# Kernel optimization log

Measured on AMD Instinct MI355X. Metric: run time of the kernel, lower is better.

Reference implementation:

```python
import jax, jax.numpy as jnp
import numpy as np

N_HEADS = 4
ROPE_THETA = 10000.0


def rotate_half(x):
    h = x.shape[-1] // 2
    return jnp.concatenate([-x[..., h:], x[..., :h]], axis=-1)


def setup_inputs() -> dict:
    key = jax.random.key(0)
    k1, k2, k3, k4, k5 = jax.random.split(key, 5)
    B, L, D, M = 4, 2048, 216, 64
    x = jax.random.normal(k1, (B, L, D), dtype=jnp.float32)
    mem_k = jax.random.normal(k2, (B, M, D), dtype=jnp.float32)
    mem_v = jax.random.normal(k3, (B, M, D), dtype=jnp.float32)
    attention_mask = jnp.ones((B, L), dtype=jnp.int32)
    # pre-transposed Linear weights (y = x @ W); scaled for stability
    Wqkv = jax.random.normal(k4, (D, 3 * D), dtype=jnp.float32) * (D ** -0.5)
    Wo = jax.random.normal(k5, (D, D), dtype=jnp.float32) * (D ** -0.5)
    return {"x": x, "mem_k": mem_k, "mem_v": mem_v,
            "attention_mask": attention_mask, "Wqkv": Wqkv, "Wo": Wo}


def reference(x, mem_k, mem_v, attention_mask, Wqkv, Wo):
    B, L, D = x.shape
    H = N_HEADS
    hd = D // H
    scale = hd ** -0.5
    M = mem_k.shape[1]

    # QKV projection -> [B, L, 3, H, hd] -> [B, H, L, hd]
    qkv = (x @ Wqkv).reshape(B, L, 3, H, hd)
    q = jnp.transpose(qkv[:, :, 0], (0, 2, 1, 3))
    k = jnp.transpose(qkv[:, :, 1], (0, 2, 1, 3))
    v = jnp.transpose(qkv[:, :, 2], (0, 2, 1, 3))

    # RoPE (cos/sin: [L, hd], broadcast over B,H)
    inv_freq = 1.0 / (ROPE_THETA ** (jnp.arange(0, hd, 2, dtype=jnp.float32) / hd))
    t = jnp.arange(L, dtype=jnp.float32)
    freqs = jnp.outer(t, inv_freq)
    emb = jnp.concatenate([freqs, freqs], axis=-1)
    cos, sin = jnp.cos(emb), jnp.sin(emb)
    q = q * cos + rotate_half(q) * sin
    k = k * cos + rotate_half(k) * sin

    # memory KV: [B, M, D] -> [B, H, M, hd], prepend along kv axis
    mk = jnp.transpose(mem_k.reshape(B, M, H, hd), (0, 2, 1, 3))
    mv = jnp.transpose(mem_v.reshape(B, M, H, hd), (0, 2, 1, 3))
    k_all = jnp.concatenate([mk, k], axis=2)  # [B, H, M+L, hd]
    v_all = jnp.concatenate([mv, v], axis=2)

    scores = jnp.einsum('bhld,bhmd->bhlm', q, k_all) * scale  # [B,H,L,M+L]

    # causal mask applies only to the self-attention block (cols >= M)
    causal = jnp.triu(jnp.ones((L, L), dtype=bool), k=1)
    full_causal = jnp.concatenate([jnp.zeros((L, M), dtype=bool), causal], axis=1)
    scores = jnp.where(full_causal[None, None], -jnp.inf, scores)

    # padding mask: memory positions always valid
    combined = jnp.concatenate(
        [jnp.ones((B, M), dtype=attention_mask.dtype), attention_mask], axis=-1)
    scores = jnp.where(combined[:, None, None, :] == 0, -jnp.inf, scores)

    attn = jax.nn.softmax(scores, axis=-1)  # dropout is identity in eval
    out = jnp.einsum('bhlm,bhmd->bhld', attn, v_all)
    out = jnp.transpose(out, (0, 2, 1, 3)).reshape(B, L, D)
    return out @ Wo
```

## Files before the change

kernel.cpp:

```cpp
#include <hip/hip_runtime.h>
#include <math.h>

#define B_ 4
#define L_ 2048
#define D_ 216
#define H_ 4
#define HD 54
#define HDP 64
#define M_ 64
#define LK 2112
#define NT_ 33
#define KP 256
#define SPB 84
#define QSCALE 0.19632593f

typedef __attribute__((ext_vector_type(8))) __bf16 bf16x8;
typedef __attribute__((ext_vector_type(4))) __bf16 bf16x4;
typedef __attribute__((ext_vector_type(4))) float f32x4;

__device__ __forceinline__ int unpack_d(int j) { return (j >> 1) + 27 * (j & 1); }

__global__ __launch_bounds__(256) void prep(const float* __restrict__ Wqkv,
                                            const float* __restrict__ Wo,
                                            const int* __restrict__ amask,
                                            const float* __restrict__ mk,
                                            const float* __restrict__ mv,
                                            __bf16* __restrict__ wqkvt,
                                            __bf16* __restrict__ wot,
                                            float2* __restrict__ table,
                                            float* __restrict__ bias,
                                            int* __restrict__ padflag,
                                            __bf16* __restrict__ kall,
                                            __bf16* __restrict__ vt) {
    const int bid = blockIdx.x, tid = threadIdx.x;
    if (bid < 768) {
        int idx = bid * 256 + tid;
        int pc = idx >> 8, k = idx & 255;
        float v = 0.f;
        if (k < 216) {
            int col = -1;
            if (pc < 256) { int h = pc >> 6, j = pc & 63;
                if (j < HD) col = h * HD + unpack_d(j); }
            else if (pc < 512) { int h = (pc - 256) >> 6, j = (pc - 256) & 63;
                if (j < HD) col = 216 + h * HD + unpack_d(j); }
            else if (pc < 728) col = 432 + (pc - 512);
            if (col >= 0) v = Wqkv[(size_t)k * 648 + col];
        }
        wqkvt[idx] = (__bf16)v;
    } else if (bid < 1024) {
        int idx = (bid - 768) * 256 + tid;
        int n = idx >> 8, k = idx & 255;
        wot[idx] = (__bf16)((n < 216 && k < 216) ? Wo[(size_t)k * 216 + n] : 0.f);
    } else if (bid < 1280) {
        int idx = (bid - 1024) * 256 + tid;
        int l = idx >> 5, ii = idx & 31;
        float2 sc = {0.f, 0.f};
        if (ii < 27) {
            float ang = (float)l * exp2f(-0.49213749924f * (float)ii);
            sc.x = sinf(ang); sc.y = cosf(ang);
        }
        table[idx] = sc;
    } else if (bid < 1313) {
        int idx = (bid - 1280) * 256 + tid;
        if (idx < B_ * LK) {
            int b = idx / LK, c = idx % LK;
            bias[idx] = (c < M_ || amask[b * L_ + c - M_] != 0) ? 0.f : -1e30f;
        }
    } else if (bid == 1313) {
        if (tid < B_ * NT_) {
            int b = tid / NT_, tile = tid % NT_;
            int flag = 0;
            for (int u = 0; u < 64; ++u) {
                int c = tile * 64 + u;
                if (c >= M_ && c < LK && amask[b * L_ + c - M_] == 0) flag = 1;
            }
            padflag[tid] = flag;
        }
    } else {
        int idx = (bid - 1314) * 256 + tid;
        int b  = idx >> 14;
        int m  = (idx >> 8) & 63;
        int h  = (idx >> 6) & 3;
        int dd = idx & 63;
        float kv = (dd < HD) ? mk[((size_t)(b * M_ + m)) * D_ + h * HD + unpack_d(dd)] : 0.f;
        kall[((size_t)(b * 4 + h) * LK + m) * HDP + dd] = (__bf16)kv;
        if (dd < HD)
            vt[((size_t)(b * 4 + h) * HD + dd) * LK + m] =
                (__bf16)mv[((size_t)(b * M_ + m)) * D_ + h * HD + dd];
    }
}

__global__ __launch_bounds__(256) void gemm_qkv(const float* __restrict__ x,
                                                const __bf16* __restrict__ Bt,
                                                const float2* __restrict__ table,
                                                __bf16* __restrict__ qb,
                                                __bf16* __restrict__ kall,
                                                __bf16* __restrict__ vt) {
    __shared__ __align__(16) __bf16 As[8192];
    __shared__ __align__(16) __bf16 Bs[4096];
    const int col0 = blockIdx.x * 64;
    const int row0 = blockIdx.y * 128;
    const int tid = threadIdx.x;
    const int lane = tid & 63;
    const int w = tid >> 6, wm = w >> 1, wn = w & 1;
    const int l15 = lane & 15, l4 = lane >> 4;

    f32x4 acc[4][2];
    #pragma unroll
    for (int m = 0; m < 4; ++m)
        #pragma unroll
        for (int n = 0; n < 2; ++n) acc[m][n] = (f32x4){0.f, 0.f, 0.f, 0.f};

    float4 rfa[4][2];
    bf16x8 rb[2];
    #pragma unroll
    for (int i = 0; i < 4; ++i) { int c = tid + 256 * i, r = c >> 3, c8 = c & 7;
        int k = c8 * 8;
        rfa[i][0] = *reinterpret_cast<const float4*>(x + (size_t)(row0 + r) * 216 + k);
        rfa[i][1] = *reinterpret_cast<const float4*>(x + (size_t)(row0 + r) * 216 + k + 4); }
    #pragma unroll
    for (int i = 0; i < 2; ++i) { int c = tid + 256 * i, r = c >> 3, c8 = c & 7;
        rb[i] = *reinterpret_cast<const bf16x8*>(Bt + (size_t)(col0 + r) * KP + c8 * 8); }

    for (int kit = 0; kit < 4; ++kit) {
        __syncthreads();
        #pragma unroll
        for (int i = 0; i < 4; ++i) { int c = tid + 256 * i, r = c >> 3, c8 = c & 7;
            bf16x8 v;
            #pragma unroll
            for (int j = 0; j < 4; ++j) { v[j] = (__bf16)rfa[i][0][j]; v[4 + j] = (__bf16)rfa[i][1][j]; }
            *reinterpret_cast<bf16x8*>(&As[r * 64 + ((c8 ^ (r & 7)) * 8)]) = v; }
        #pragma unroll
        for (int i = 0; i < 2; ++i) { int c = tid + 256 * i, r = c >> 3, c8 = c & 7;
            *reinterpret_cast<bf16x8*>(&Bs[r * 64 + ((c8 ^ (r & 7)) * 8)]) = rb[i]; }
        __syncthreads();
        if (kit < 3) {
            const int k0 = (kit + 1) * 64;
            #pragma unroll
            for (int i = 0; i < 4; ++i) { int c = tid + 256 * i, r = c >> 3, c8 = c & 7;
                int k = k0 + c8 * 8;
                if (k < 216) {
                    rfa[i][0] = *reinterpret_cast<const float4*>(x + (size_t)(row0 + r) * 216 + k);
                    rfa[i][1] = *reinterpret_cast<const float4*>(x + (size_t)(row0 + r) * 216 + k + 4);
                } else {
                    rfa[i][0] = (float4){0.f, 0.f, 0.f, 0.f};
                    rfa[i][1] = (float4){0.f, 0.f, 0.f, 0.f};
                } }
            #pragma unroll
            for (int i = 0; i < 2; ++i) { int c = tid + 256 * i, r = c >> 3, c8 = c & 7;
                rb[i] = *reinterpret_cast<const bf16x8*>(Bt + (size_t)(col0 + r) * KP + k0 + c8 * 8); }
        }
        #pragma unroll
        for (int ks = 0; ks < 2; ++ks) {
            bf16x8 af[4], bfr[2];
            #pragma unroll
            for (int m = 0; m < 4; ++m) { int row = wm * 64 + m * 16 + l15; int ch = ks * 4 + l4;
                af[m] = *reinterpret_cast<const bf16x8*>(&As[row * 64 + ((ch ^ (row & 7)) * 8)]); }
            #pragma unroll
            for (int n = 0; n < 2; ++n) { int row = wn * 32 + n * 16 + l15; int ch = ks * 4 + l4;
                bfr[n] = *reinterpret_cast<const bf16x8*>(&Bs[row * 64 + ((ch ^ (row & 7)) * 8)]); }
            #pragma unroll
            for (int m = 0; m < 4; ++m)
                #pragma unroll
                for (int n = 0; n < 2; ++n)
                    acc[m][n] = __builtin_amdgcn_mfma_f32_16x16x32_bf16(af[m], bfr[n], acc[m][n], 0, 0, 0);
        }
    }

    #pragma unroll
    for (int m = 0; m < 4; ++m)
        #pragma unroll
        for (int n = 0; n < 2; ++n) {
            const int cc = col0 + wn * 32 + n * 16 + l15;
            const int rowb = row0 + wm * 64 + m * 16 + l4 * 4;
            const int b = rowb >> 11;
            const int lbase = rowb & 2047;
            if (cc < 512) {
                const bool isq = cc < 256;
                const int h = (cc >> 6) & 3, j = cc & 63;
                const int half = j & 1, ii = j >> 1;
                #pragma unroll
                for (int rr = 0; rr < 4; ++rr) {
                    float me = acc[m][n][rr];
                    float pr = __shfl_xor(me, 1);
                    float2 sc = table[(lbase + rr) * 32 + ii];
                    float v = me * sc.y + (half ? pr * sc.x : -pr * sc.x);
                    if (isq) {
                        qb[((size_t)(b * 4 + h) * L_ + lbase + rr) * HDP + j] =
                            (__bf16)(v * QSCALE);
                    } else {
                        kall[((size_t)(b * 4 + h) * LK + M_ + lbase + rr) * HDP + j] =
                            (__bf16)v;
                    }
                }
            } else if (cc < 728) {
                const int dp = cc - 512;
                const int h = (dp * 1214) >> 16;
                const int d = dp - h * 54;
                #pragma unroll
                for (int rr = 0; rr < 4; ++rr)
                    vt[((size_t)(b * 4 + h) * HD + d) * LK + M_ + lbase + rr] =
                        (__bf16)acc[m][n][rr];
            }
        }
}

__global__ __launch_bounds__(256) void gemm_out(const __bf16* __restrict__ A,
                                                const __bf16* __restrict__ Bt,
                                                float* __restrict__ C, int N) {
    __shared__ __align__(16) __bf16 As[8192];
    __shared__ __align__(16) __bf16 Bs[4096];
    const int col0 = blockIdx.x * 64;
    const int row0 = blockIdx.y * 128;
    const int tid = threadIdx.x;
    const int lane = tid & 63;
    const int w = tid >> 6, wm = w >> 1, wn = w & 1;
    const int l15 = lane & 15, l4 = lane >> 4;

    f32x4 acc[4][2];
    #pragma unroll
    for (int m = 0; m < 4; ++m)
        #pragma unroll
        for (int n = 0; n < 2; ++n) acc[m][n] = (f32x4){0.f, 0.f, 0.f, 0.f};

    bf16x8 ra[4], rb[2];
    #pragma unroll
    for (int i = 0; i < 4; ++i) { int c = tid + 256 * i, r = c >> 3, c8 = c & 7;
        ra[i] = *reinterpret_cast<const bf16x8*>(A + (size_t)(row0 + r) * KP + c8 * 8); }
    #pragma unroll
    for (int i = 0; i < 2; ++i) { int c = tid + 256 * i, r = c >> 3, c8 = c & 7;
        rb[i] = *reinterpret_cast<const bf16x8*>(Bt + (size_t)(col0 + r) * KP + c8 * 8); }

    for (int kit = 0; kit < 4; ++kit) {
        __syncthreads();
        #pragma unroll
        for (int i = 0; i < 4; ++i) { int c = tid + 256 * i, r = c >> 3, c8 = c & 7;
            *reinterpret_cast<bf16x8*>(&As[r * 64 + ((c8 ^ (r & 7)) * 8)]) = ra[i]; }
        #pragma unroll
        for (int i = 0; i < 2; ++i) { int c = tid + 256 * i, r = c >> 3, c8 = c & 7;
            *reinterpret_cast<bf16x8*>(&Bs[r * 64 + ((c8 ^ (r & 7)) * 8)]) = rb[i]; }
        __syncthreads();
        if (kit < 3) {
            const int k0 = (kit + 1) * 64;
            #pragma unroll
            for (int i = 0; i < 4; ++i) { int c = tid + 256 * i, r = c >> 3, c8 = c & 7;
                ra[i] = *reinterpret_cast<const bf16x8*>(A + (size_t)(row0 + r) * KP + k0 + c8 * 8); }
            #pragma unroll
            for (int i = 0; i < 2; ++i) { int c = tid + 256 * i, r = c >> 3, c8 = c & 7;
                rb[i] = *reinterpret_cast<const bf16x8*>(Bt + (size_t)(col0 + r) * KP + k0 + c8 * 8); }
        }
        #pragma unroll
        for (int ks = 0; ks < 2; ++ks) {
            bf16x8 af[4], bfr[2];
            #pragma unroll
            for (int m = 0; m < 4; ++m) { int row = wm * 64 + m * 16 + l15; int ch = ks * 4 + l4;
                af[m] = *reinterpret_cast<const bf16x8*>(&As[row * 64 + ((ch ^ (row & 7)) * 8)]); }
            #pragma unroll
            for (int n = 0; n < 2; ++n) { int row = wn * 32 + n * 16 + l15; int ch = ks * 4 + l4;
                bfr[n] = *reinterpret_cast<const bf16x8*>(&Bs[row * 64 + ((ch ^ (row & 7)) * 8)]); }
            #pragma unroll
            for (int m = 0; m < 4; ++m)
                #pragma unroll
                for (int n = 0; n < 2; ++n)
                    acc[m][n] = __builtin_amdgcn_mfma_f32_16x16x32_bf16(af[m], bfr[n], acc[m][n], 0, 0, 0);
        }
    }
    #pragma unroll
    for (int m = 0; m < 4; ++m)
        #pragma unroll
        for (int n = 0; n < 2; ++n) {
            int cc = col0 + wn * 32 + n * 16 + l15;
            if (cc < N) {
                #pragma unroll
                for (int rr = 0; rr < 4; ++rr)
                    C[(size_t)(row0 + wm * 64 + m * 16 + l4 * 4 + rr) * N + cc] = acc[m][n][rr];
            }
        }
}

__global__ __launch_bounds__(256) void flash_split(const __bf16* __restrict__ qb,
                                                   const __bf16* __restrict__ kall,
                                                   const __bf16* __restrict__ vt,
                                                   const float* __restrict__ bias,
                                                   const int* __restrict__ padflag,
                                                   float* __restrict__ op,
                                                   float* __restrict__ ml) {
    int qt = 31, sp = 0;
    {
        int sidx = blockIdx.x, accq = 0;
        for (int q = 0; q < 32; ++q) {
            int c = (q + 9) >> 3;
            if (sidx < accq + c) { qt = q; sp = sidx - accq; break; }
            accq += c;
        }
    }
    const int pb = blockIdx.y * SPB + blockIdx.x;
    const int q0 = qt * 64;
    const int bh = blockIdx.y;
    const int b = bh >> 2;
    const int tstart = sp * 8;
    const int tend = min(tstart + 8, qt + 2);

    __shared__ __align__(16) __bf16 Qs[4096];
    __shared__ __align__(16) __bf16 Ks[2][4096];
    __shared__ __align__(16) __bf16 Vs[2][4096];
    __shared__ __align__(16) __bf16 Ps[4096];
    __shared__ float biasS[2][64];

    const int tid = threadIdx.x;
    const int lane = tid & 63;
    const int w = tid >> 6;
    const int l15 = lane & 15;
    const int l4 = lane >> 4;

    {
        const __bf16* src = qb + ((size_t)bh * L_ + q0) * HDP;
        for (int ch = tid; ch < 512; ch += 256) {
            int row = ch >> 3, c8 = ch & 7;
            bf16x8 v = *reinterpret_cast<const bf16x8*>(src + ch * 8);
            *reinterpret_cast<bf16x8*>(&Qs[row * 64 + ((c8 ^ (row & 7)) * 8)]) = v;
        }
        if (tid < 160) {
            int buf = tid >= 80, q = tid - 80 * buf;
            int d = 54 + (q >> 3), c8 = q & 7;
            bf16x8 z{};
            *reinterpret_cast<bf16x8*>(&Vs[buf][d * 64 + ((c8 ^ (d & 7)) * 8)]) = z;
        }
    }

    const int rq = q0 + 16 * w + l15;
    const __bf16* kbase = kall + (size_t)bh * LK * HDP;
    const __bf16* vbase = vt + (size_t)bh * HD * LK;

    bf16x8 rk[2], rv[2];
    float biasR = 0.f;
    {
        const __bf16* ks = kbase + (size_t)tstart * 64 * HDP;
        rk[0] = *reinterpret_cast<const bf16x8*>(ks + tid * 8);
        rk[1] = *reinterpret_cast<const bf16x8*>(ks + (tid + 256) * 8);
        { int d = tid >> 3, c8 = tid & 7;
          rv[0] = *reinterpret_cast<const bf16x8*>(vbase + (size_t)d * LK + tstart * 64 + c8 * 8); }
        if (tid < 176) { int c = tid + 256, d = c >> 3, c8 = c & 7;
          rv[1] = *reinterpret_cast<const bf16x8*>(vbase + (size_t)d * LK + tstart * 64 + c8 * 8); }
        if (tid < 64) biasR = bias[b * LK + tstart * 64 + tid];

        { int r = tid >> 3, c8 = tid & 7;
          *reinterpret_cast<bf16x8*>(&Ks[0][r * 64 + ((c8 ^ (r & 7)) * 8)]) = rk[0]; }
        { int c = tid + 256, r = c >> 3, c8 = c & 7;
          *reinterpret_cast<bf16x8*>(&Ks[0][r * 64 + ((c8 ^ (r & 7)) * 8)]) = rk[1]; }
        { int d = tid >> 3, c8 = tid & 7;
          *reinterpret_cast<bf16x8*>(&Vs[0][d * 64 + ((c8 ^ (d & 7)) * 8)]) = rv[0]; }
        if (tid < 176) { int c = tid + 256, d = c >> 3, c8 = c & 7;
          *reinterpret_cast<bf16x8*>(&Vs[0][d * 64 + ((c8 ^ (d & 7)) * 8)]) = rv[1]; }
        if (tid < 64) biasS[0][tid] = biasR;
    }
    if (tstart + 1 < tend) {
        const __bf16* ks = kbase + (size_t)(tstart + 1) * 64 * HDP;
        rk[0] = *reinterpret_cast<const bf16x8*>(ks + tid * 8);
        rk[1] = *reinterpret_cast<const bf16x8*>(ks + (tid + 256) * 8);
        { int d = tid >> 3, c8 = tid & 7;
          rv[0] = *reinterpret_cast<const bf16x8*>(vbase + (size_t)d * LK + (tstart + 1) * 64 + c8 * 8); }
        if (tid < 176) { int c = tid + 256, d = c >> 3, c8 = c & 7;
          rv[1] = *reinterpret_cast<const bf16x8*>(vbase + (size_t)d * LK + (tstart + 1) * 64 + c8 * 8); }
        if (tid < 64) biasR = bias[b * LK + (tstart + 1) * 64 + tid];
    }

    __syncthreads();
    bf16x8 aQ[2];
    {
        int qrow = 16 * w + l15, s = (qrow & 7) << 3;
        aQ[0] = *reinterpret_cast<const bf16x8*>(&Qs[qrow * 64 + ((l4 * 8) ^ s)]);
        aQ[1] = *reinterpret_cast<const bf16x8*>(&Qs[qrow * 64 + ((32 + l4 * 8) ^ s)]);
    }

    f32x4 Oacc[4];
    #pragma unroll
    for (int nt = 0; nt < 4; ++nt) Oacc[nt] = (f32x4){0.f, 0.f, 0.f, 0.f};
    float m_run = -1e30f, l_run = 0.f;

    int p = 0;
    for (int t = tstart; t < tend; ++t) {
        const int cbase = t * 64;
        const int qbuf = p ^ 1;
        if (t + 1 < tend) {
            { int r = tid >> 3, c8 = tid & 7;
              *reinterpret_cast<bf16x8*>(&Ks[qbuf][r * 64 + ((c8 ^ (r & 7)) * 8)]) = rk[0]; }
            { int c = tid + 256, r = c >> 3, c8 = c & 7;
              *reinterpret_cast<bf16x8*>(&Ks[qbuf][r * 64 + ((c8 ^ (r & 7)) * 8)]) = rk[1]; }
            { int d = tid >> 3, c8 = tid & 7;
              *reinterpret_cast<bf16x8*>(&Vs[qbuf][d * 64 + ((c8 ^ (d & 7)) * 8)]) = rv[0]; }
            if (tid < 176) { int c = tid + 256, d = c >> 3, c8 = c & 7;
              *reinterpret_cast<bf16x8*>(&Vs[qbuf][d * 64 + ((c8 ^ (d & 7)) * 8)]) = rv[1]; }
            if (tid < 64) biasS[qbuf][tid] = biasR;
        }
        if (t + 2 < tend) {
            const __bf16* ks = kbase + (size_t)(cbase + 128) * HDP;
            rk[0] = *reinterpret_cast<const bf16x8*>(ks + tid * 8);
            rk[1] = *reinterpret_cast<const bf16x8*>(ks + (tid + 256) * 8);
            { int d = tid >> 3, c8 = tid & 7;
              rv[0] = *reinterpret_cast<const bf16x8*>(vbase + (size_t)d * LK + cbase + 128 + c8 * 8); }
            if (tid < 176) { int c = tid + 256, d = c >> 3, c8 = c & 7;
              rv[1] = *reinterpret_cast<const bf16x8*>(vbase + (size_t)d * LK + cbase + 128 + c8 * 8); }
            if (tid < 64) biasR = bias[b * LK + cbase + 128 + tid];
        }
        const int flag = padflag[b * NT_ + t];

        f32x4 S[4];
        #pragma unroll
        for (int nt = 0; nt < 4; ++nt) {
            int krow = nt * 16 + l15, s = (krow & 7) << 3;
            bf16x8 b0 = *reinterpret_cast<const bf16x8*>(&Ks[p][krow * 64 + ((l4 * 8) ^ s)]);
            bf16x8 b1 = *reinterpret_cast<const bf16x8*>(&Ks[p][krow * 64 + ((32 + l4 * 8) ^ s)]);
            f32x4 acc = (f32x4){0.f, 0.f, 0.f, 0.f};
            acc = __builtin_amdgcn_mfma_f32_16x16x32_bf16(b0, aQ[0], acc, 0, 0, 0);
            acc = __builtin_amdgcn_mfma_f32_16x16x32_bf16(b1, aQ[1], acc, 0, 0, 0);
            S[nt] = acc;
        }
        if (flag) {
            #pragma unroll
            for (int nt = 0; nt < 4; ++nt)
                #pragma unroll
                for (int r = 0; r < 4; ++r)
                    S[nt][r] += biasS[p][nt * 16 + l4 * 4 + r];
        }
        if (t == qt + 1) {
            #pragma unroll
            for (int nt = 0; nt < 4; ++nt)
                #pragma unroll
                for (int r = 0; r < 4; ++r) {
                    int cg = cbase + nt * 16 + l4 * 4 + r;
                    if (cg > rq + M_) S[nt][r] = -1e30f;
                }
        }
        float mx;
        {
            float a0 = fmaxf(fmaxf(S[0][0], S[0][1]), S[0][2]);
            float a1 = fmaxf(fmaxf(S[0][3], S[1][0]), S[1][1]);
            float a2 = fmaxf(fmaxf(S[1][2], S[1][3]), S[2][0]);
            float a3 = fmaxf(fmaxf(S[2][1], S[2][2]), S[2][3]);
            float a4 = fmaxf(fmaxf(S[3][0], S[3][1]), S[3][2]);
            float b0 = fmaxf(fmaxf(a0, a1), a2);
            float b1 = fmaxf(fmaxf(a3, a4), S[3][3]);
            mx = fmaxf(b0, b1);
        }
        mx = fmaxf(mx, __shfl_xor(mx, 16));
        mx = fmaxf(mx, __shfl_xor(mx, 32));
        if (!__all(mx <= m_run + 8.f)) {
            float m_new = fmaxf(m_run, mx);
            float alpha = exp2f(m_run - m_new);
            m_run = m_new;
            l_run *= alpha;
            #pragma unroll
            for (int nt = 0; nt < 4; ++nt)
                #pragma unroll
                for (int r = 0; r < 4; ++r) Oacc[nt][r] *= alpha;
        }
        float ls = 0.f;
        #pragma unroll
        for (int nt = 0; nt < 4; ++nt)
            #pragma unroll
            for (int r = 0; r < 4; ++r) {
                float pv = exp2f(S[nt][r] - m_run);
                S[nt][r] = pv;
                ls += pv;
            }
        ls += __shfl_xor(ls, 16);
        ls += __shfl_xor(ls, 32);
        l_run += ls;
        {
            int prow = 16 * w + l15, s = (prow & 7) << 3;
            #pragma unroll
            for (int nt = 0; nt < 4; ++nt) {
                bf16x4 pk;
                pk[0] = (__bf16)S[nt][0]; pk[1] = (__bf16)S[nt][1];
                pk[2] = (__bf16)S[nt][2]; pk[3] = (__bf16)S[nt][3];
                *reinterpret_cast<bf16x4*>(&Ps[prow * 64 + ((nt * 16 + l4 * 4) ^ s)]) = pk;
            }
        }
        bf16x8 aP[2];
        {
            int prow = 16 * w + l15, s = (prow & 7) << 3;
            aP[0] = *reinterpret_cast<const bf16x8*>(&Ps[prow * 64 + ((l4 * 8) ^ s)]);
            aP[1] = *reinterpret_cast<const bf16x8*>(&Ps[prow * 64 + ((32 + l4 * 8) ^ s)]);
        }
        #pragma unroll
        for (int nt = 0; nt < 4; ++nt) {
            int vrow = nt * 16 + l15, s = (vrow & 7) << 3;
            bf16x8 v0 = *reinterpret_cast<const bf16x8*>(&Vs[p][vrow * 64 + ((l4 * 8) ^ s)]);
            bf16x8 v1 = *reinterpret_cast<const bf16x8*>(&Vs[p][vrow * 64 + ((32 + l4 * 8) ^ s)]);
            Oacc[nt] = __builtin_amdgcn_mfma_f32_16x16x32_bf16(v0, aP[0], Oacc[nt], 0, 0, 0);
            Oacc[nt] = __builtin_amdgcn_mfma_f32_16x16x32_bf16(v1, aP[1], Oacc[nt], 0, 0, 0);
        }
        __syncthreads();
        p ^= 1;
    }

    if (l4 == 0) {
        ml[((size_t)pb * 64 + 16 * w + l15) * 2 + 0] = m_run;
        ml[((size_t)pb * 64 + 16 * w + l15) * 2 + 1] = l_run;
    }
    #pragma unroll
    for (int nt = 0; nt < 4; ++nt) {
        #pragma unroll
        for (int r = 0; r < 4; ++r) {
            int d = nt * 16 + l4 * 4 + r;
            if (d < HD)
                op[((size_t)pb * HD + d) * 64 + 16 * w + l15] = Oacc[nt][r];
        }
    }
}

__global__ __launch_bounds__(256) void combine(const float* __restrict__ op,
                                               const float* __restrict__ ml,
                                               __bf16* __restrict__ aoutb) {
    const int qt = blockIdx.x, bh = blockIdx.y;
    const int b = bh >> 2, h = bh & 3;
    const int ns = (qt + 9) >> 3;
    int accq = 0;
    for (int q = 0; q < qt; ++q) accq += (q + 9) >> 3;
    const int pb0 = bh * SPB + accq;
    const int row = threadIdx.x & 63;
    const int dseg = threadIdx.x >> 6;

    float mi[5], li[5];
    float m = -1e30f;
    for (int i = 0; i < ns; ++i) {
        mi[i] = ml[((size_t)(pb0 + i) * 64 + row) * 2 + 0];
        li[i] = ml[((size_t)(pb0 + i) * 64 + row) * 2 + 1];
        m = fmaxf(m, mi[i]);
    }
    float wgt[5], Lr = 0.f;
    for (int i = 0; i < ns; ++i) {
        wgt[i] = exp2f(mi[i] - m);
        Lr += li[i] * wgt[i];
    }
    float inv = 1.f / Lr;
    #pragma unroll
    for (int j = 0; j < 14; ++j) {
        int d = dseg * 14 + j;
        if (d < HD) {
            float o = 0.f;
            for (int i = 0; i < ns; ++i)
                o += wgt[i] * op[((size_t)(pb0 + i) * HD + d) * 64 + row];
            aoutb[((size_t)(b * L_) + qt * 64 + row) * KP + h * HD + d] = (__bf16)(o * inv);
        }
    }
}

extern "C" void kernel_launch(void* const* d_in, const int* in_sizes, int n_in,
                              void* d_out, int out_size, void* d_ws, size_t ws_size,
                              hipStream_t stream) {
    const float* x     = (const float*)d_in[0];
    const float* mem_k = (const float*)d_in[1];
    const float* mem_v = (const float*)d_in[2];
    const int*   amask = (const int*)d_in[3];
    const float* Wqkv  = (const float*)d_in[4];
    const float* Wo    = (const float*)d_in[5];
    float* out = (float*)d_out;

    char* p = (char*)d_ws;
    float* bias    = (float*)p;        p += (size_t)B_ * LK * 4;
    int*   padflag = (int*)p;          p += (size_t)B_ * NT_ * 4;
    float2* table  = (float2*)p;       p += (size_t)2048 * 32 * 8;
    __bf16* wqkvt  = (__bf16*)p;       p += (size_t)768 * KP * 2;
    __bf16* wot    = (__bf16*)p;       p += (size_t)256 * KP * 2;
    __bf16* aoutb  = (__bf16*)p;       p += (size_t)8192 * KP * 2;
    __bf16* qb     = (__bf16*)p;       p += (size_t)16 * 2048 * 64 * 2;
    __bf16* kall   = (__bf16*)p;       p += (size_t)16 * 2112 * 64 * 2;
    __bf16* vt     = (__bf16*)p;       p += (size_t)16 * 54 * 2112 * 2;
    float* opbuf   = (float*)p;        p += (size_t)16 * SPB * HD * 64 * 4;
    float* mlbuf   = (float*)p;        p += (size_t)16 * SPB * 64 * 2 * 4;

    prep<<<dim3(1570), 256, 0, stream>>>(Wqkv, Wo, amask, mem_k, mem_v,
                                         wqkvt, wot, table, bias, padflag, kall, vt);
    gemm_qkv<<<dim3(12, 64), 256, 0, stream>>>(x, wqkvt, table, qb, kall, vt);
    flash_split<<<dim3(SPB, 16), 256, 0, stream>>>(qb, kall, vt, bias, padflag,
                                                   opbuf, mlbuf);
    combine<<<dim3(32, 16), 256, 0, stream>>>(opbuf, mlbuf, aoutb);
    gemm_out<<<dim3(4, 64), 256, 0, stream>>>(aoutb, wot, out, 216);
}
```

Measured before the change: 98.54 us.

## Balance flash split ranges, write single-split tiles directly, raise MFMA priority

Query tiles whose KV range fits in one split now normalize and write bf16 output straight to the attention output buffer. This lets the combine kernel skip the first seven tiles and avoids their partial round-trip through global memory. Split KV ranges are now divided evenly rather than in fixed chunks of eight, which balances work between the splits of a tile. MFMA sections are wrapped in s_setprio to favour matrix issue over other waves.

```diff
diff --git a/kernel.cpp b/kernel.cpp
--- a/kernel.cpp
+++ b/kernel.cpp
@@ -284,7 +284,8 @@
                                                    const float* __restrict__ bias,
                                                    const int* __restrict__ padflag,
                                                    float* __restrict__ op,
-                                                   float* __restrict__ ml) {
+                                                   float* __restrict__ ml,
+                                                   __bf16* __restrict__ aoutb) {
     int qt = 31, sp = 0;
     {
         int sidx = blockIdx.x, accq = 0;
@@ -297,9 +298,13 @@
     const int pb = blockIdx.y * SPB + blockIdx.x;
     const int q0 = qt * 64;
     const int bh = blockIdx.y;
-    const int b = bh >> 2;
-    const int tstart = sp * 8;
-    const int tend = min(tstart + 8, qt + 2);
+    const int b = bh >> 2, h = bh & 3;
+    const int ntl = qt + 2;
+    const int ns = (ntl + 7) >> 3;
+    const int base = ntl / ns, rem = ntl % ns;
+    const int tstart = sp * base + min(sp, rem);
+    const int tend = tstart + base + (sp < rem ? 1 : 0);
+    const bool single = (ns == 1);
 
     __shared__ __align__(16) __bf16 Qs[4096];
     __shared__ __align__(16) __bf16 Ks[2][4096];
@@ -406,6 +411,7 @@
         const int flag = padflag[b * NT_ + t];
 
         f32x4 S[4];
+        __builtin_amdgcn_s_setprio(1);
         #pragma unroll
         for (int nt = 0; nt < 4; ++nt) {
             int krow = nt * 16 + l15, s = (krow & 7) << 3;
@@ -416,6 +422,7 @@
             acc = __builtin_amdgcn_mfma_f32_16x16x32_bf16(b1, aQ[1], acc, 0, 0, 0);
             S[nt] = acc;
         }
+        __builtin_amdgcn_s_setprio(0);
         if (flag) {
             #pragma unroll
             for (int nt = 0; nt < 4; ++nt)
@@ -483,6 +490,7 @@
             aP[0] = *reinterpret_cast<const bf16x8*>(&Ps[prow * 64 + ((l4 * 8) ^ s)]);
             aP[1] = *reinterpret_cast<const bf16x8*>(&Ps[prow * 64 + ((32 + l4 * 8) ^ s)]);
         }
+        __builtin_amdgcn_s_setprio(1);
         #pragma unroll
         for (int nt = 0; nt < 4; ++nt) {
             int vrow = nt * 16 + l15, s = (vrow & 7) << 3;
@@ -491,21 +499,36 @@
             Oacc[nt] = __builtin_amdgcn_mfma_f32_16x16x32_bf16(v0, aP[0], Oacc[nt], 0, 0, 0);
             Oacc[nt] = __builtin_amdgcn_mfma_f32_16x16x32_bf16(v1, aP[1], Oacc[nt], 0, 0, 0);
         }
+        __builtin_amdgcn_s_setprio(0);
         __syncthreads();
         p ^= 1;
     }
 
-    if (l4 == 0) {
-        ml[((size_t)pb * 64 + 16 * w + l15) * 2 + 0] = m_run;
-        ml[((size_t)pb * 64 + 16 * w + l15) * 2 + 1] = l_run;
-    }
-    #pragma unroll
-    for (int nt = 0; nt < 4; ++nt) {
-        #pragma unroll
-        for (int r = 0; r < 4; ++r) {
-            int d = nt * 16 + l4 * 4 + r;
-            if (d < HD)
-                op[((size_t)pb * HD + d) * 64 + 16 * w + l15] = Oacc[nt][r];
+    if (single) {
+        float inv = 1.f / l_run;
+        const size_t rowbase = (size_t)b * L_ + q0 + 16 * w + l15;
+        #pragma unroll
+        for (int nt = 0; nt < 4; ++nt) {
+            #pragma unroll
+            for (int r = 0; r < 4; ++r) {
+                int d = nt * 16 + l4 * 4 + r;
+                if (d < HD)
+                    aoutb[rowbase * KP + h * HD + d] = (__bf16)(Oacc[nt][r] * inv);
+            }
+        }
+    } else {
+        if (l4 == 0) {
+            ml[((size_t)pb * 64 + 16 * w + l15) * 2 + 0] = m_run;
+            ml[((size_t)pb * 64 + 16 * w + l15) * 2 + 1] = l_run;
+        }
+        #pragma unroll
+        for (int nt = 0; nt < 4; ++nt) {
+            #pragma unroll
+            for (int r = 0; r < 4; ++r) {
+                int d = nt * 16 + l4 * 4 + r;
+                if (d < HD)
+                    op[((size_t)pb * HD + d) * 64 + 16 * w + l15] = Oacc[nt][r];
+            }
         }
     }
 }
@@ -513,7 +536,7 @@
 __global__ __launch_bounds__(256) void combine(const float* __restrict__ op,
                                                const float* __restrict__ ml,
                                                __bf16* __restrict__ aoutb) {
-    const int qt = blockIdx.x, bh = blockIdx.y;
+    const int qt = blockIdx.x + 7, bh = blockIdx.y;
     const int b = bh >> 2, h = bh & 3;
     const int ns = (qt + 9) >> 3;
     int accq = 0;
@@ -575,7 +598,7 @@
                                          wqkvt, wot, table, bias, padflag, kall, vt);
     gemm_qkv<<<dim3(12, 64), 256, 0, stream>>>(x, wqkvt, table, qb, kall, vt);
     flash_split<<<dim3(SPB, 16), 256, 0, stream>>>(qb, kall, vt, bias, padflag,
-                                                   opbuf, mlbuf);
-    combine<<<dim3(32, 16), 256, 0, stream>>>(opbuf, mlbuf, aoutb);
+                                                   opbuf, mlbuf, aoutb);
+    combine<<<dim3(25, 16), 256, 0, stream>>>(opbuf, mlbuf, aoutb);
     gemm_out<<<dim3(4, 64), 256, 0, stream>>>(aoutb, wot, out, 216);
 }
```

Measured after the change: 98.83 us. No clear change (+0.3%).
